# Optimization experiments

Measured on AMD Instinct MI355X. Metric: run time of the kernel, lower is better.

Reference implementation:

```python
import jax, jax.numpy as jnp
import numpy as np

N_NODES = 100000
N_EDGES = 1600000
IN_DIM = 128
HIDDEN = 128


def setup_inputs() -> dict:
    key = jax.random.key(0)
    k1, k2, k3 = jax.random.split(key, 3)
    x = jax.random.normal(k1, (N_NODES, IN_DIM), dtype=jnp.float32)
    edge_index = jax.random.randint(k2, (2, N_EDGES), 0, N_NODES, dtype=jnp.int64)
    # Glorot-ish init for the GCN weight
    W = jax.random.normal(k3, (IN_DIM, HIDDEN), dtype=jnp.float32) * (1.0 / np.sqrt(IN_DIM))
    b = jnp.zeros((HIDDEN,), dtype=jnp.float32)
    return {"x": x, "edge_index": edge_index, "W": W, "b": b}


def reference(x, edge_index, W, b):
    N = x.shape[0]
    # PyG GCNConv: add self-loops, symmetric deg^{-1/2} normalization,
    # linear transform, scatter-add aggregation at destination, + bias.
    loop = jnp.arange(N, dtype=edge_index.dtype)
    src = jnp.concatenate([edge_index[0], loop])
    dst = jnp.concatenate([edge_index[1], loop])

    ones = jnp.ones(src.shape[0], dtype=x.dtype)
    deg = jax.ops.segment_sum(ones, dst, num_segments=N)  # in-degree incl. self-loop
    dinv = jnp.where(deg > 0, jax.lax.rsqrt(deg), 0.0)
    norm = dinv[src] * dinv[dst]  # [E+N]

    xw = x @ W  # [N, H] dense transform first (GCNConv default)
    msgs = xw[src] * norm[:, None]  # gather + scale, [E+N, H]
    out = jax.ops.segment_sum(msgs, dst, num_segments=N) + b  # scatter-add
    return jax.nn.relu(out)
```

## Files before the change

kernel.cpp:

```cpp
#include <hip/hip_runtime.h>
#include <hip/hip_bf16.h>


#define SCAN_BLK 256
#define NP1 128
#define MAXB 1024

typedef short  short8 __attribute__((ext_vector_type(8)));
typedef float  f32x4  __attribute__((ext_vector_type(4)));

__device__ inline unsigned short f2b(float f) {
    unsigned u = __float_as_uint(f);
    return (unsigned short)((u + 0x7fffu + ((u >> 16) & 1u)) >> 16);
}

__device__ inline void acc4(float4& a, uint2 u) {
    a.x += __uint_as_float(u.x << 16);
    a.y += __uint_as_float(u.x & 0xffff0000u);
    a.z += __uint_as_float(u.y << 16);
    a.w += __uint_as_float(u.y & 0xffff0000u);
}

__global__ __launch_bounds__(256) void k_hist(const int* __restrict__ dst,
                                              int* __restrict__ hist,
                                              int E, int B, int chunk) {
    __shared__ int h[MAXB];
    for (int i = threadIdx.x; i < B; i += 256) h[i] = 0;
    __syncthreads();
    int e0 = blockIdx.x * chunk;
    int e1 = min(E, e0 + chunk);
    for (int e = e0 + threadIdx.x; e < e1; e += 256)
        atomicAdd(&h[dst[e] >> 7], 1);
    __syncthreads();
    for (int i = threadIdx.x; i < B; i += 256)
        hist[i * NP1 + blockIdx.x] = h[i];
}

__global__ __launch_bounds__(SCAN_BLK) void k_scanA(const int* __restrict__ in,
                                                    int* __restrict__ bsum, int M) {
    __shared__ int s[SCAN_BLK];
    int t = threadIdx.x;
    int i = blockIdx.x * SCAN_BLK + t;
    s[t] = (i < M) ? in[i] : 0;
    __syncthreads();
    for (int off = SCAN_BLK / 2; off > 0; off >>= 1) {
        if (t < off) s[t] += s[t + off];
        __syncthreads();
    }
    if (t == 0) bsum[blockIdx.x] = s[0];
}

__global__ __launch_bounds__(512) void k_scanB(int* __restrict__ bsum, int nb) {
    __shared__ int s[512];
    int t = threadIdx.x;
    int v = (t < nb) ? bsum[t] : 0;
    s[t] = v;
    __syncthreads();
    for (int off = 1; off < 512; off <<= 1) {
        int add = (t >= off) ? s[t - off] : 0;
        __syncthreads();
        s[t] += add;
        __syncthreads();
    }
    if (t < nb) bsum[t] = s[t] - v;
}

__global__ __launch_bounds__(SCAN_BLK) void k_scanC2(const int* __restrict__ in,
                                                     const int* __restrict__ bsum,
                                                     int* __restrict__ outp, int M) {
    __shared__ int s[SCAN_BLK];
    int t = threadIdx.x;
    int i = blockIdx.x * SCAN_BLK + t;
    int v = (i < M) ? in[i] : 0;
    s[t] = v;
    __syncthreads();
    for (int off = 1; off < SCAN_BLK; off <<= 1) {
        int add = (t >= off) ? s[t - off] : 0;
        __syncthreads();
        s[t] += add;
        __syncthreads();
    }
    if (i < M) outp[i] = s[t] - v + bsum[blockIdx.x];
}

__global__ __launch_bounds__(256) void k_scatter(const int* __restrict__ src,
                                                 const int* __restrict__ dst,
                                                 const int* __restrict__ hist_s,
                                                 unsigned* __restrict__ bucketed,
                                                 int E, int B, int chunk) {
    __shared__ int cur[MAXB];
    for (int i = threadIdx.x; i < B; i += 256)
        cur[i] = hist_s[i * NP1 + blockIdx.x];
    __syncthreads();
    int e0 = blockIdx.x * chunk;
    int e1 = min(E, e0 + chunk);
    for (int e = e0 + threadIdx.x; e < e1; e += 256) {
        int d = dst[e];
        int p = atomicAdd(&cur[d >> 7], 1);
        bucketed[p] = (unsigned)src[e] | ((unsigned)(d & 127) << 17);
    }
}

__global__ __launch_bounds__(256) void k_csr(const unsigned* __restrict__ bucketed,
                                             const int* __restrict__ hist_s,
                                             int* __restrict__ csr_src,
                                             int* __restrict__ deg_g,
                                             int* __restrict__ rowstart_g,
                                             float* __restrict__ dinv_g,
                                             int E, int B, int N) {
    const int b = blockIdx.x;
    const int t = threadIdx.x;
    const int base = hist_s[b * NP1];
    const int endv = (b + 1 < B) ? hist_s[(b + 1) * NP1] : E;
    const int cnt = endv - base;
    const int node0 = b << 7;

    __shared__ int sdeg[128], sscan[128], cur[128];
    if (t < 128) sdeg[t] = 0;
    __syncthreads();
    for (int i = t; i < cnt; i += 256)
        atomicAdd(&sdeg[bucketed[base + i] >> 17], 1);
    __syncthreads();
    if (t < 128) sscan[t] = sdeg[t];
    __syncthreads();
    for (int off = 1; off < 128; off <<= 1) {
        int add = 0;
        if (t < 128 && t >= off) add = sscan[t - off];
        __syncthreads();
        if (t < 128) sscan[t] += add;
        __syncthreads();
    }
    if (t < 128) {
        int rs = sscan[t] - sdeg[t];
        cur[t] = rs;
        int node = node0 + t;
        if (node < N) {
            deg_g[node] = sdeg[t];
            rowstart_g[node] = base + rs;
            dinv_g[node] = rsqrtf((float)(sdeg[t] + 1));
        }
    }
    __syncthreads();
    for (int i = t; i < cnt; i += 256) {
        unsigned w = bucketed[base + i];
        int p = atomicAdd(&cur[w >> 17], 1);
        csr_src[base + p] = (int)(w & 0x1FFFFu);
    }
}

__global__ __launch_bounds__(256) void k_wconv(const float* __restrict__ W,
                                               unsigned short* __restrict__ Wt) {
    int i = blockIdx.x * 256 + threadIdx.x;
    int k = i >> 7, n = i & 127;
    Wt[n * 128 + k] = f2b(W[k * 128 + n]);
}

__global__ __launch_bounds__(256) void k_gemm(const float* __restrict__ x,
                                              const unsigned short* __restrict__ Wt,
                                              const float* __restrict__ dinv,
                                              unsigned* __restrict__ xs_out, int N) {
    __shared__ short out_lds[4][16][136];
    const int t = threadIdx.x;
    const int wv = t >> 6;
    const int lane = t & 63;
    const int quad = lane >> 4;
    const int lid = lane & 15;
    const int row0 = blockIdx.x * 64;

    int grow = row0 + wv * 16 + lid;
    int growc = grow < N ? grow : N - 1;
    short8 af[4];
#pragma unroll
    for (int q = 0; q < 4; ++q) {
        const float4* xr = (const float4*)(x + (size_t)growc * 128 + q * 32 + quad * 8);
        float4 f0 = xr[0], f1 = xr[1];
        af[q][0] = (short)f2b(f0.x); af[q][1] = (short)f2b(f0.y);
        af[q][2] = (short)f2b(f0.z); af[q][3] = (short)f2b(f0.w);
        af[q][4] = (short)f2b(f1.x); af[q][5] = (short)f2b(f1.y);
        af[q][6] = (short)f2b(f1.z); af[q][7] = (short)f2b(f1.w);
    }

    int drow = row0 + wv * 16 + quad * 4;
    float4 dv4;
    if (drow + 3 < N)      dv4 = *(const float4*)(dinv + drow);
    else {
        dv4.x = dinv[min(drow + 0, N - 1)];
        dv4.y = dinv[min(drow + 1, N - 1)];
        dv4.z = dinv[min(drow + 2, N - 1)];
        dv4.w = dinv[min(drow + 3, N - 1)];
    }

#pragma unroll
    for (int c = 0; c < 8; ++c) {
        f32x4 acc = {0.f, 0.f, 0.f, 0.f};
#pragma unroll
        for (int q = 0; q < 4; ++q) {
            const short8* bp = (const short8*)(Wt + (size_t)(c * 16 + lid) * 128 +
                                               q * 32 + quad * 8);
            acc = __builtin_amdgcn_mfma_f32_16x16x32_bf16(af[q], *bp, acc, 0, 0, 0);
        }
        out_lds[wv][quad * 4 + 0][c * 16 + lid] = (short)f2b(acc[0] * dv4.x);
        out_lds[wv][quad * 4 + 1][c * 16 + lid] = (short)f2b(acc[1] * dv4.y);
        out_lds[wv][quad * 4 + 2][c * 16 + lid] = (short)f2b(acc[2] * dv4.z);
        out_lds[wv][quad * 4 + 3][c * 16 + lid] = (short)f2b(acc[3] * dv4.w);
    }
    __syncthreads();

    int rl = lane >> 2;
    int cseg = lane & 3;
    int grow2 = row0 + wv * 16 + rl;
    if (grow2 < N) {
        uint4* dstp = (uint4*)(xs_out + (size_t)grow2 * 64);
        const uint4* srcp = (const uint4*)((const char*)&out_lds[wv][rl][0] + cseg * 64);
#pragma unroll
        for (int tt = 0; tt < 4; ++tt) dstp[cseg * 4 + tt] = srcp[tt];
    }
}

__global__ __launch_bounds__(256) void k_aggregate(const unsigned* __restrict__ xs,
                                                   const int* __restrict__ csr_src,
                                                   const int* __restrict__ rowstart,
                                                   const int* __restrict__ deg,
                                                   const float* __restrict__ dinv,
                                                   const float* __restrict__ bias,
                                                   float* __restrict__ out, int N) {
    const int wave = threadIdx.x >> 6;
    const int lane = threadIdx.x & 63;
    const int n = blockIdx.x * 4 + wave;
    if (n >= N) return;

    const int rs = rowstart[n];
    const int c = deg[n];
    const float dv = dinv[n];
    const int half = lane >> 5;
    const int sub = lane & 31;

    int idxreg = (lane < c) ? csr_src[rs + lane] : n;

    float4 acc = make_float4(0.f, 0.f, 0.f, 0.f);
    const uint2* xsv = (const uint2*)xs;

    int cmain = c < 64 ? c : 64;
    int i = 0;
    for (; i + 16 <= cmain; i += 16) {
#pragma unroll
        for (int j = 0; j < 8; ++j) {
            int row = __shfl(idxreg, i + 2 * j + half);
            uint2 u = xsv[(size_t)row * 32 + sub];
            acc4(acc, u);
        }
    }
    if (i < cmain) {
#pragma unroll
        for (int j = 0; j < 8; ++j) {
            int e = i + 2 * j + half;
            int row = __shfl(idxreg, e < 64 ? e : 0);
            uint2 u = xsv[(size_t)row * 32 + sub];
            if (e >= cmain) { u.x = 0u; u.y = 0u; }
            acc4(acc, u);
        }
        i = cmain;
    }
    for (; i < c; i += 2) {
        int e = i + half;
        uint2 u = make_uint2(0u, 0u);
        if (e < c) u = xsv[(size_t)csr_src[rs + e] * 32 + sub];
        acc4(acc, u);
    }

    acc.x += __shfl_xor(acc.x, 32);
    acc.y += __shfl_xor(acc.y, 32);
    acc.z += __shfl_xor(acc.z, 32);
    acc.w += __shfl_xor(acc.w, 32);

    if (lane < 32) {
        uint2 su = xsv[(size_t)n * 32 + lane];
        acc4(acc, su);
        float4 bb = ((const float4*)bias)[lane];
        float4 o;
        o.x = fmaxf(dv * acc.x + bb.x, 0.f);
        o.y = fmaxf(dv * acc.y + bb.y, 0.f);
        o.z = fmaxf(dv * acc.z + bb.z, 0.f);
        o.w = fmaxf(dv * acc.w + bb.w, 0.f);
        ((float4*)(out + (size_t)n * 128))[lane] = o;
    }
}

extern "C" void kernel_launch(void* const* d_in, const int* in_sizes, int n_in,
                              void* d_out, int out_size, void* d_ws, size_t ws_size,
                              hipStream_t stream) {
    const float* x   = (const float*)d_in[0];
    const int*   ei  = (const int*)d_in[1];
    const float* W   = (const float*)d_in[2];
    const float* b   = (const float*)d_in[3];
    float*       out = (float*)d_out;

    const int N = in_sizes[0] / 128;
    const int E = in_sizes[1] / 2;
    const int* src = ei;
    const int* dst = ei + E;

    const int B = (N + 127) >> 7;
    const int M = B * NP1;
    const int chunk = (E + NP1 - 1) / NP1;

    auto align = [](size_t v) { return (v + 255) & ~(size_t)255; };
    char* p = (char*)d_ws;
    int*            hist     = (int*)p;            p += align((size_t)M * 4);
    int*            hist_s   = (int*)p;            p += align((size_t)M * 4);
    int*            bsum     = (int*)p;            p += align(512 * 4);
    int*            deg      = (int*)p;            p += align((size_t)N * 4);
    int*            rowstart = (int*)p;            p += align((size_t)N * 4);
    float*          dinv     = (float*)p;          p += align((size_t)N * 4);
    unsigned*       bucketed = (unsigned*)p;       p += align((size_t)E * 4);
    int*            csr_src  = (int*)p;            p += align((size_t)E * 4);
    unsigned*       xs       = (unsigned*)p;       p += align((size_t)N * 64 * 4);
    unsigned short* Wt       = (unsigned short*)p; p += align(128 * 128 * 2);
    (void)ws_size;

    const int nbM = (M + SCAN_BLK - 1) / SCAN_BLK;

    k_hist   <<<NP1, 256, 0, stream>>>(dst, hist, E, B, chunk);
    k_scanA  <<<nbM, 256, 0, stream>>>(hist, bsum, M);
    k_scanB  <<<1, 512, 0, stream>>>(bsum, nbM);
    k_scanC2 <<<nbM, 256, 0, stream>>>(hist, bsum, hist_s, M);
    k_scatter<<<NP1, 256, 0, stream>>>(src, dst, hist_s, bucketed, E, B, chunk);
    k_csr    <<<B, 256, 0, stream>>>(bucketed, hist_s, csr_src, deg, rowstart, dinv,
                                     E, B, N);
    k_wconv  <<<64, 256, 0, stream>>>(W, Wt);
    k_gemm   <<<(N + 63) / 64, 256, 0, stream>>>(x, Wt, dinv, xs, N);
    k_aggregate<<<(N + 3) / 4, 256, 0, stream>>>(xs, csr_src, rowstart, deg, dinv, b,
                                                 out, N);
}
```

Before: 266.5 us.

## Process four nodes per wave with 16-byte gathers; fuse W conversion into histogram

The aggregation kernel now handles four destination nodes per wavefront. Each lane group gathers 16-byte chunks instead of 8-byte ones, so each neighbor row is read by 16 lanes and four edges are in flight per iteration. Degree and rowstart arrays are merged into a single CSR rowptr, and the scan now writes in place. The weight transpose/convert is folded into the histogram kernel, removing one launch. The per-node loop over four nodes is sequential within a wave, so it may cut latency hiding per node, and there are more cross-lane reductions.

```diff
diff --git a/kernel.cpp b/kernel.cpp
--- a/kernel.cpp
+++ b/kernel.cpp
@@ -14,15 +14,17 @@
     return (unsigned short)((u + 0x7fffu + ((u >> 16) & 1u)) >> 16);
 }
 
-__device__ inline void acc4(float4& a, uint2 u) {
-    a.x += __uint_as_float(u.x << 16);
-    a.y += __uint_as_float(u.x & 0xffff0000u);
-    a.z += __uint_as_float(u.y << 16);
-    a.w += __uint_as_float(u.y & 0xffff0000u);
+__device__ inline void acc4(float4& a, unsigned lo, unsigned hi) {
+    a.x += __uint_as_float(lo << 16);
+    a.y += __uint_as_float(lo & 0xffff0000u);
+    a.z += __uint_as_float(hi << 16);
+    a.w += __uint_as_float(hi & 0xffff0000u);
 }
 
 __global__ __launch_bounds__(256) void k_hist(const int* __restrict__ dst,
                                               int* __restrict__ hist,
+                                              const float* __restrict__ W,
+                                              unsigned short* __restrict__ Wt,
                                               int E, int B, int chunk) {
     __shared__ int h[MAXB];
     for (int i = threadIdx.x; i < B; i += 256) h[i] = 0;
@@ -34,6 +36,11 @@
     __syncthreads();
     for (int i = threadIdx.x; i < B; i += 256)
         hist[i * NP1 + blockIdx.x] = h[i];
+    if (blockIdx.x < 64) {
+        int i = blockIdx.x * 256 + threadIdx.x;
+        int k = i >> 7, n = i & 127;
+        Wt[n * 128 + k] = f2b(W[k * 128 + n]);
+    }
 }
 
 __global__ __launch_bounds__(SCAN_BLK) void k_scanA(const int* __restrict__ in,
@@ -65,13 +72,13 @@
     if (t < nb) bsum[t] = s[t] - v;
 }
 
-__global__ __launch_bounds__(SCAN_BLK) void k_scanC2(const int* __restrict__ in,
+__global__ __launch_bounds__(SCAN_BLK) void k_scanC2(int* __restrict__ data,
                                                      const int* __restrict__ bsum,
-                                                     int* __restrict__ outp, int M) {
+                                                     int M) {
     __shared__ int s[SCAN_BLK];
     int t = threadIdx.x;
     int i = blockIdx.x * SCAN_BLK + t;
-    int v = (i < M) ? in[i] : 0;
+    int v = (i < M) ? data[i] : 0;
     s[t] = v;
     __syncthreads();
     for (int off = 1; off < SCAN_BLK; off <<= 1) {
@@ -80,7 +87,7 @@
         s[t] += add;
         __syncthreads();
     }
-    if (i < M) outp[i] = s[t] - v + bsum[blockIdx.x];
+    if (i < M) data[i] = s[t] - v + bsum[blockIdx.x];
 }
 
 __global__ __launch_bounds__(256) void k_scatter(const int* __restrict__ src,
@@ -104,8 +111,7 @@
 __global__ __launch_bounds__(256) void k_csr(const unsigned* __restrict__ bucketed,
                                              const int* __restrict__ hist_s,
                                              int* __restrict__ csr_src,
-                                             int* __restrict__ deg_g,
-                                             int* __restrict__ rowstart_g,
+                                             int* __restrict__ rowptr,
                                              float* __restrict__ dinv_g,
                                              int E, int B, int N) {
     const int b = blockIdx.x;
@@ -135,24 +141,17 @@
         cur[t] = rs;
         int node = node0 + t;
         if (node < N) {
-            deg_g[node] = sdeg[t];
-            rowstart_g[node] = base + rs;
+            rowptr[node] = base + rs;
             dinv_g[node] = rsqrtf((float)(sdeg[t] + 1));
         }
     }
+    if (b == B - 1 && t == 0) rowptr[N] = E;
     __syncthreads();
     for (int i = t; i < cnt; i += 256) {
         unsigned w = bucketed[base + i];
         int p = atomicAdd(&cur[w >> 17], 1);
         csr_src[base + p] = (int)(w & 0x1FFFFu);
     }
-}
-
-__global__ __launch_bounds__(256) void k_wconv(const float* __restrict__ W,
-                                               unsigned short* __restrict__ Wt) {
-    int i = blockIdx.x * 256 + threadIdx.x;
-    int k = i >> 7, n = i & 127;
-    Wt[n * 128 + k] = f2b(W[k * 128 + n]);
 }
 
 __global__ __launch_bounds__(256) void k_gemm(const float* __restrict__ x,
@@ -217,72 +216,86 @@
     }
 }
 
-__global__ __launch_bounds__(256) void k_aggregate(const unsigned* __restrict__ xs,
+__global__ __launch_bounds__(256) void k_aggregate(const uint4* __restrict__ xs4,
                                                    const int* __restrict__ csr_src,
-                                                   const int* __restrict__ rowstart,
-                                                   const int* __restrict__ deg,
+                                                   const int* __restrict__ rowptr,
                                                    const float* __restrict__ dinv,
                                                    const float* __restrict__ bias,
                                                    float* __restrict__ out, int N) {
     const int wave = threadIdx.x >> 6;
     const int lane = threadIdx.x & 63;
-    const int n = blockIdx.x * 4 + wave;
-    if (n >= N) return;
-
-    const int rs = rowstart[n];
-    const int c = deg[n];
-    const float dv = dinv[n];
-    const int half = lane >> 5;
-    const int sub = lane & 31;
-
-    int idxreg = (lane < c) ? csr_src[rs + lane] : n;
-
-    float4 acc = make_float4(0.f, 0.f, 0.f, 0.f);
-    const uint2* xsv = (const uint2*)xs;
-
-    int cmain = c < 64 ? c : 64;
-    int i = 0;
-    for (; i + 16 <= cmain; i += 16) {
-#pragma unroll
-        for (int j = 0; j < 8; ++j) {
-            int row = __shfl(idxreg, i + 2 * j + half);
-            uint2 u = xsv[(size_t)row * 32 + sub];
-            acc4(acc, u);
+    const int g0 = (blockIdx.x * 4 + wave) * 4;
+    if (g0 >= N) return;
+    const int grp = lane >> 4;
+    const int sub = lane & 15;
+
+    int   rp  = rowptr[min(g0 + min(lane, 4), N)];
+    float dvl = dinv[min(g0 + min(lane, 3), N - 1)];
+
+    int rs[4], c[4], idx[4];
+#pragma unroll
+    for (int k = 0; k < 4; ++k) {
+        rs[k] = __shfl(rp, k);
+        c[k]  = __shfl(rp, k + 1) - rs[k];
+    }
+#pragma unroll
+    for (int k = 0; k < 4; ++k)
+        idx[k] = (lane < c[k]) ? csr_src[rs[k] + lane] : 0;
+
+    const uint2* xs2 = (const uint2*)xs4;
+
+#pragma unroll
+    for (int k = 0; k < 4; ++k) {
+        int n = g0 + k;
+        if (n < N) {
+            const int cc = c[k];
+            float4 a0 = make_float4(0.f, 0.f, 0.f, 0.f);
+            float4 a1 = make_float4(0.f, 0.f, 0.f, 0.f);
+            int cmain = cc < 64 ? cc : 64;
+            int jmax = (cmain + 3) >> 2;
+            for (int j = 0; j < jmax; ++j) {
+                int e = j * 4 + grp;
+                int row = __shfl(idx[k], e & 63);
+                uint4 u = xs4[(size_t)row * 16 + sub];
+                if (e >= cc) { u.x = 0u; u.y = 0u; u.z = 0u; u.w = 0u; }
+                acc4(a0, u.x, u.y);
+                acc4(a1, u.z, u.w);
+            }
+            for (int e0 = 64; e0 < cc; e0 += 4) {
+                int e = e0 + grp;
+                uint4 u = make_uint4(0u, 0u, 0u, 0u);
+                if (e < cc) {
+                    int row = csr_src[rs[k] + e];
+                    u = xs4[(size_t)row * 16 + sub];
+                }
+                acc4(a0, u.x, u.y);
+                acc4(a1, u.z, u.w);
+            }
+            a0.x += __shfl_xor(a0.x, 16); a0.x += __shfl_xor(a0.x, 32);
+            a0.y += __shfl_xor(a0.y, 16); a0.y += __shfl_xor(a0.y, 32);
+            a0.z += __shfl_xor(a0.z, 16); a0.z += __shfl_xor(a0.z, 32);
+            a0.w += __shfl_xor(a0.w, 16); a0.w += __shfl_xor(a0.w, 32);
+            a1.x += __shfl_xor(a1.x, 16); a1.x += __shfl_xor(a1.x, 32);
+            a1.y += __shfl_xor(a1.y, 16); a1.y += __shfl_xor(a1.y, 32);
+            a1.z += __shfl_xor(a1.z, 16); a1.z += __shfl_xor(a1.z, 32);
+            a1.w += __shfl_xor(a1.w, 16); a1.w += __shfl_xor(a1.w, 32);
+
+            if (lane < 32) {
+                int p = lane >> 4;
+                int f4 = (lane & 15) * 2 + p;
+                float4 av = p ? a1 : a0;
+                uint2 su = xs2[(size_t)n * 32 + f4];
+                acc4(av, su.x, su.y);
+                float dv = __shfl(dvl, k);
+                float4 bb = ((const float4*)bias)[f4];
+                float4 o;
+                o.x = fmaxf(dv * av.x + bb.x, 0.f);
+                o.y = fmaxf(dv * av.y + bb.y, 0.f);
+                o.z = fmaxf(dv * av.z + bb.z, 0.f);
+                o.w = fmaxf(dv * av.w + bb.w, 0.f);
+                ((float4*)(out + (size_t)n * 128))[f4] = o;
+            }
         }
-    }
-    if (i < cmain) {
-#pragma unroll
-        for (int j = 0; j < 8; ++j) {
-            int e = i + 2 * j + half;
-            int row = __shfl(idxreg, e < 64 ? e : 0);
-            uint2 u = xsv[(size_t)row * 32 + sub];
-            if (e >= cmain) { u.x = 0u; u.y = 0u; }
-            acc4(acc, u);
-        }
-        i = cmain;
-    }
-    for (; i < c; i += 2) {
-        int e = i + half;
-        uint2 u = make_uint2(0u, 0u);
-        if (e < c) u = xsv[(size_t)csr_src[rs + e] * 32 + sub];
-        acc4(acc, u);
-    }
-
-    acc.x += __shfl_xor(acc.x, 32);
-    acc.y += __shfl_xor(acc.y, 32);
-    acc.z += __shfl_xor(acc.z, 32);
-    acc.w += __shfl_xor(acc.w, 32);
-
-    if (lane < 32) {
-        uint2 su = xsv[(size_t)n * 32 + lane];
-        acc4(acc, su);
-        float4 bb = ((const float4*)bias)[lane];
-        float4 o;
-        o.x = fmaxf(dv * acc.x + bb.x, 0.f);
-        o.y = fmaxf(dv * acc.y + bb.y, 0.f);
-        o.z = fmaxf(dv * acc.z + bb.z, 0.f);
-        o.w = fmaxf(dv * acc.w + bb.w, 0.f);
-        ((float4*)(out + (size_t)n * 128))[lane] = o;
     }
 }
 
@@ -307,10 +320,8 @@
     auto align = [](size_t v) { return (v + 255) & ~(size_t)255; };
     char* p = (char*)d_ws;
     int*            hist     = (int*)p;            p += align((size_t)M * 4);
-    int*            hist_s   = (int*)p;            p += align((size_t)M * 4);
     int*            bsum     = (int*)p;            p += align(512 * 4);
-    int*            deg      = (int*)p;            p += align((size_t)N * 4);
-    int*            rowstart = (int*)p;            p += align((size_t)N * 4);
+    int*            rowptr   = (int*)p;            p += align(((size_t)N + 1) * 4);
     float*          dinv     = (float*)p;          p += align((size_t)N * 4);
     unsigned*       bucketed = (unsigned*)p;       p += align((size_t)E * 4);
     int*            csr_src  = (int*)p;            p += align((size_t)E * 4);
@@ -320,15 +331,13 @@
 
     const int nbM = (M + SCAN_BLK - 1) / SCAN_BLK;
 
-    k_hist   <<<NP1, 256, 0, stream>>>(dst, hist, E, B, chunk);
+    k_hist   <<<NP1, 256, 0, stream>>>(dst, hist, W, Wt, E, B, chunk);
     k_scanA  <<<nbM, 256, 0, stream>>>(hist, bsum, M);
     k_scanB  <<<1, 512, 0, stream>>>(bsum, nbM);
-    k_scanC2 <<<nbM, 256, 0, stream>>>(hist, bsum, hist_s, M);
-    k_scatter<<<NP1, 256, 0, stream>>>(src, dst, hist_s, bucketed, E, B, chunk);
-    k_csr    <<<B, 256, 0, stream>>>(bucketed, hist_s, csr_src, deg, rowstart, dinv,
-                                     E, B, N);
-    k_wconv  <<<64, 256, 0, stream>>>(W, Wt);
+    k_scanC2 <<<nbM, 256, 0, stream>>>(hist, bsum, M);
+    k_scatter<<<NP1, 256, 0, stream>>>(src, dst, hist, bucketed, E, B, chunk);
+    k_csr    <<<B, 256, 0, stream>>>(bucketed, hist, csr_src, rowptr, dinv, E, B, N);
     k_gemm   <<<(N + 63) / 64, 256, 0, stream>>>(x, Wt, dinv, xs, N);
-    k_aggregate<<<(N + 3) / 4, 256, 0, stream>>>(xs, csr_src, rowstart, deg, dinv, b,
-                                                 out, N);
-}
+    k_aggregate<<<(N + 15) / 16, 256, 0, stream>>>((const uint4*)xs, csr_src, rowptr,
+                                                   dinv, b, out, N);
+}
```

New measurement: 261.7 us. Within noise of the previous version (-1.8%).
